# Performance work log

Measured on AMD Instinct MI355X. Metric: run time of the kernel, lower is better.

The kernel has to match this reference:

```python
import jax, jax.numpy as jnp
import numpy as np

NUM_NODES = 500000
DIM = 128
BATCH = 131072
MOMENTUM = 0.9


def setup_inputs() -> dict:
    key = jax.random.key(0)
    ks = jax.random.split(key, 6)
    s = 1.0 / np.sqrt(DIM)
    return {
        "hidden": jax.random.normal(ks[0], (NUM_NODES, DIM), jnp.float32),
        "variance": jnp.ones((NUM_NODES, DIM), jnp.float32),
        "idx": jnp.arange(BATCH, dtype=jnp.int64 if jax.config.jax_enable_x64 else jnp.int32),
        "new_repr": jax.random.normal(ks[1], (BATCH, DIM), jnp.float32),
        "W_ih": jax.random.normal(ks[2], (3 * DIM, DIM), jnp.float32) * s,
        "W_hh": jax.random.normal(ks[3], (3 * DIM, DIM), jnp.float32) * s,
        "b_ih": jax.random.normal(ks[4], (3 * DIM,), jnp.float32) * s,
        "b_hh": jax.random.normal(ks[5], (3 * DIM,), jnp.float32) * s,
    }


def _gru_cell(x, h, W_ih, W_hh, b_ih, b_hh):
    # torch GRUCell gate layout: [reset | update | new], each of size DIM
    gi = x @ W_ih.T + b_ih          # [B, 3*DIM]
    gh = h @ W_hh.T + b_hh          # [B, 3*DIM]
    gi_r, gi_z, gi_n = jnp.split(gi, 3, axis=-1)
    gh_r, gh_z, gh_n = jnp.split(gh, 3, axis=-1)
    r = jax.nn.sigmoid(gi_r + gh_r)
    z = jax.nn.sigmoid(gi_z + gh_z)
    n = jnp.tanh(gi_n + r * gh_n)
    return (1.0 - z) * n + z * h


def reference(hidden, variance, idx, new_repr, W_ih, W_hh, b_ih, b_hh):
    h_prev = hidden[idx]                                   # gather [B, DIM]
    h_new = _gru_cell(new_repr, h_prev, W_ih, W_hh, b_ih, b_hh)
    delta = h_new - h_prev
    var_new = MOMENTUM * variance[idx] + (1.0 - MOMENTUM) * delta * delta
    hidden_out = hidden.at[idx].set(h_new)                 # scatter write
    variance_out = variance.at[idx].set(var_new)
    return jnp.stack([hidden_out, variance_out])           # [2, N, DIM]
```

## Files before the change

### kernel.cpp

```cpp
#include <hip/hip_runtime.h>
#include <hip/hip_bf16.h>
#include <cstdint>
#include <cstddef>

#define NUM_NODES 500000
#define DIM 128
#define BATCH 131072
#define NBLK (NUM_NODES / 32)

typedef __attribute__((ext_vector_type(8))) short short8;
typedef __attribute__((ext_vector_type(4))) short short4_t;
typedef __attribute__((ext_vector_type(4))) float f32x4;

static __device__ __forceinline__ short f2bf(float f) {
    unsigned u = __builtin_bit_cast(unsigned, f);
    u += 0x7fffu + ((u >> 16) & 1u);
    return (short)(u >> 16);
}
static __device__ __forceinline__ float bf2f(short s) {
    unsigned u = ((unsigned)(unsigned short)s) << 16;
    return __builtin_bit_cast(float, u);
}
static __device__ __forceinline__ f32x4 ntl(const float* p) {
    return __builtin_nontemporal_load((const f32x4*)p);
}
static __device__ __forceinline__ void nts(float* p, f32x4 v) {
    __builtin_nontemporal_store(v, (f32x4*)p);
}

__global__ void k_init(int* __restrict__ inv,
                       unsigned char* __restrict__ mask,
                       const float* __restrict__ Wih,
                       const float* __restrict__ Whh,
                       short* __restrict__ WbIH,
                       short* __restrict__ WbHH) {
    int i = blockIdx.x * blockDim.x + threadIdx.x;
    if (i < NUM_NODES) {
        if (inv)  inv[i] = -1;
        if (mask) mask[i] = 0;
    }
    if (i < 3 * DIM * DIM) {
        WbIH[i] = f2bf(Wih[i]);
        WbHH[i] = f2bf(Whh[i]);
    }
}

__global__ void k_scatter(int* __restrict__ inv, unsigned char* __restrict__ mask,
                          const int* __restrict__ idx) {
    int i = blockIdx.x * blockDim.x + threadIdx.x;
    if (i < BATCH) {
        int n = idx[i];
        if (inv)  inv[n] = i;
        if (mask) mask[n] = 1;
    }
}

__global__ void __launch_bounds__(512)
k_stream(const float* __restrict__ hidden,
         const float* __restrict__ variance,
         const int*   __restrict__ inv,
         const float* __restrict__ xg,
         const short* __restrict__ WbIH,
         const short* __restrict__ WbHH,
         const float* __restrict__ b_ih,
         const float* __restrict__ b_hh,
         float* __restrict__ out0,
         float* __restrict__ out1) {
    __shared__ __align__(16) char smem[26112];
    short (*Xb)[136] = (short(*)[136])smem;
    short (*Hb)[136] = (short(*)[136])(smem + 8704);
    short (*Vb)[136] = (short(*)[136])(smem + 17408);
    short (*Hn)[136] = (short(*)[136])smem;
    __shared__ int rinfo[32];
    __shared__ int hasUpd;

    const int t  = threadIdx.x;
    const int pb = (int)(((unsigned)blockIdx.x * 4099u) % 15625u);
    const int rb = pb * 32;

    if (t == 0) hasUpd = 0;
    if (t < 32) rinfo[t] = inv[rb + t];
    __syncthreads();
    if (t < 32 && rinfo[t] >= 0) hasUpd = 1;
    __syncthreads();

    if (!hasUpd) {
        #pragma unroll
        for (int jj = 0; jj < 2; ++jj) {
            int j = t + jj * 512;
            size_t off = (size_t)rb * DIM + j * 4;
            f32x4 h = ntl(hidden + off);
            f32x4 v = ntl(variance + off);
            nts(out0 + off, h);
            nts(out1 + off, v);
        }
        return;
    }

    #pragma unroll
    for (int jj = 0; jj < 2; ++jj) {
        int j = t + jj * 512;
        int row = j >> 5, c4 = j & 31;
        size_t off = (size_t)(rb + row) * DIM + c4 * 4;
        f32x4 hv = ntl(hidden + off);
        f32x4 vv = ntl(variance + off);
        int iv = rinfo[row];
        f32x4 xv = {0.f, 0.f, 0.f, 0.f};
        if (iv >= 0) {
            xv = ntl(xg + (size_t)iv * DIM + c4 * 4);
        } else {
            nts(out0 + off, hv);
            nts(out1 + off, vv);
        }
        short4_t xs, hs, vs;
        xs.x = f2bf(xv.x); xs.y = f2bf(xv.y); xs.z = f2bf(xv.z); xs.w = f2bf(xv.w);
        hs.x = f2bf(hv.x); hs.y = f2bf(hv.y); hs.z = f2bf(hv.z); hs.w = f2bf(hv.w);
        vs.x = f2bf(vv.x); vs.y = f2bf(vv.y); vs.z = f2bf(vv.z); vs.w = f2bf(vv.w);
        *(short4_t*)&Xb[row][c4 * 4] = xs;
        *(short4_t*)&Hb[row][c4 * 4] = hs;
        *(short4_t*)&Vb[row][c4 * 4] = vs;
    }
    __syncthreads();

    const int w  = t >> 6;
    const int l  = t & 63;
    const int c  = l & 15;
    const int gq = l >> 4;

    float sr[2][4], sz[2][4], gin[2][4], ghn[2][4];

    #pragma unroll
    for (int th = 0; th < 3; ++th) {
        f32x4 acc[2][2] = {};
        const int o = w * 16 + th * 128 + c;
        #pragma unroll
        for (int ks = 0; ks < 4; ++ks) {
            const int k0 = ks * 32 + gq * 8;
            const short8 aX0 = *(const short8*)&Xb[c][k0];
            const short8 aX1 = *(const short8*)&Xb[16 + c][k0];
            const short8 aH0 = *(const short8*)&Hb[c][k0];
            const short8 aH1 = *(const short8*)&Hb[16 + c][k0];
            const short8 bi = *(const short8*)(WbIH + (size_t)o * DIM + k0);
            const short8 bh = *(const short8*)(WbHH + (size_t)o * DIM + k0);
            acc[0][0] = __builtin_amdgcn_mfma_f32_16x16x32_bf16(aX0, bi, acc[0][0], 0, 0, 0);
            acc[1][0] = __builtin_amdgcn_mfma_f32_16x16x32_bf16(aX1, bi, acc[1][0], 0, 0, 0);
            acc[0][1] = __builtin_amdgcn_mfma_f32_16x16x32_bf16(aH0, bh, acc[0][1], 0, 0, 0);
            acc[1][1] = __builtin_amdgcn_mfma_f32_16x16x32_bf16(aH1, bh, acc[1][1], 0, 0, 0);
        }
        #pragma unroll
        for (int mt = 0; mt < 2; ++mt)
            #pragma unroll
            for (int r = 0; r < 4; ++r) {
                if (th == 0) sr[mt][r]  = acc[mt][0][r] + acc[mt][1][r];
                if (th == 1) sz[mt][r]  = acc[mt][0][r] + acc[mt][1][r];
                if (th == 2) { gin[mt][r] = acc[mt][0][r]; ghn[mt][r] = acc[mt][1][r]; }
            }
    }
    __syncthreads();

    const int d = w * 16 + c;
    const float bs_r = b_ih[d]       + b_hh[d];
    const float bs_z = b_ih[d + 128] + b_hh[d + 128];
    const float bi_n = b_ih[d + 256];
    const float bh_n = b_hh[d + 256];

    #pragma unroll
    for (int mt = 0; mt < 2; ++mt) {
        #pragma unroll
        for (int r = 0; r < 4; ++r) {
            const int m = mt * 16 + gq * 4 + r;
            float s_r  = sr[mt][r] + bs_r;
            float s_z  = sz[mt][r] + bs_z;
            float gi_n = gin[mt][r] + bi_n;
            float gh_n = ghn[mt][r] + bh_n;
            float rg = 1.f / (1.f + __expf(-s_r));
            float zg = 1.f / (1.f + __expf(-s_z));
            float aa = gi_n + rg * gh_n;
            float n  = 1.f - 2.f / (__expf(2.f * aa) + 1.f);
            float h  = bf2f(Hb[m][d]);
            Hn[m][d] = f2bf((1.f - zg) * n + zg * h);
        }
    }
    __syncthreads();

    #pragma unroll
    for (int jj = 0; jj < 2; ++jj) {
        int j = t + jj * 512;
        int row = j >> 5, c4 = j & 31;
        if (rinfo[row] < 0) continue;
        size_t off = (size_t)(rb + row) * DIM + c4 * 4;
        short4_t hns = *(short4_t*)&Hn[row][c4 * 4];
        short4_t hs  = *(short4_t*)&Hb[row][c4 * 4];
        short4_t vs  = *(short4_t*)&Vb[row][c4 * 4];
        f32x4 hn, var;
        hn.x = bf2f(hns.x); hn.y = bf2f(hns.y); hn.z = bf2f(hns.z); hn.w = bf2f(hns.w);
        float dx = hn.x - bf2f(hs.x), dy = hn.y - bf2f(hs.y);
        float dz = hn.z - bf2f(hs.z), dw = hn.w - bf2f(hs.w);
        var.x = 0.9f * bf2f(vs.x) + 0.1f * dx * dx;
        var.y = 0.9f * bf2f(vs.y) + 0.1f * dy * dy;
        var.z = 0.9f * bf2f(vs.z) + 0.1f * dz * dz;
        var.w = 0.9f * bf2f(vs.w) + 0.1f * dw * dw;
        nts(out0 + off, hn);
        nts(out1 + off, var);
    }
}

__global__ void __launch_bounds__(256)
k_copy(const float* __restrict__ hidden,
       const float* __restrict__ variance,
       const unsigned char* __restrict__ mask,
       float* __restrict__ out0,
       float* __restrict__ out1) {
    int gid = blockIdx.x * 256 + threadIdx.x;
    int row = gid >> 4;
    int c8  = gid & 15;
    if (mask && mask[row]) return;
    size_t off = (size_t)row * DIM + c8 * 8;
    f32x4 a0 = *(const f32x4*)(hidden + off);
    f32x4 a1 = *(const f32x4*)(hidden + off + 4);
    f32x4 b0 = *(const f32x4*)(variance + off);
    f32x4 b1 = *(const f32x4*)(variance + off + 4);
    *(f32x4*)(out0 + off)     = a0;
    *(f32x4*)(out0 + off + 4) = a1;
    *(f32x4*)(out1 + off)     = b0;
    *(f32x4*)(out1 + off + 4) = b1;
}

__global__ void __launch_bounds__(512)
k_gru(const float* __restrict__ hidden,
      const float* __restrict__ variance,
      const int*   __restrict__ idx,
      const float* __restrict__ xg,
      const short* __restrict__ WbIH,
      const short* __restrict__ WbHH,
      const float* __restrict__ b_ih,
      const float* __restrict__ b_hh,
      float* __restrict__ out0,
      float* __restrict__ out1) {
    __shared__ __align__(16) char smem[26112];
    short (*Xb)[136] = (short(*)[136])smem;
    short (*Hb)[136] = (short(*)[136])(smem + 8704);
    short (*Vb)[136] = (short(*)[136])(smem + 17408);
    short (*Hn)[136] = (short(*)[136])smem;

    const int t  = threadIdx.x;
    const int rb = blockIdx.x * 32;

    #pragma unroll
    for (int jj = 0; jj < 2; ++jj) {
        int j = t + jj * 512;
        int row = j >> 5, c4 = j & 31;
        int node = idx[rb + row];
        f32x4 xv = *(const f32x4*)(xg + (size_t)(rb + row) * DIM + c4 * 4);
        f32x4 hv = *(const f32x4*)(hidden + (size_t)node * DIM + c4 * 4);
        f32x4 vv = *(const f32x4*)(variance + (size_t)node * DIM + c4 * 4);
        short4_t xs, hs, vs;
        xs.x = f2bf(xv.x); xs.y = f2bf(xv.y); xs.z = f2bf(xv.z); xs.w = f2bf(xv.w);
        hs.x = f2bf(hv.x); hs.y = f2bf(hv.y); hs.z = f2bf(hv.z); hs.w = f2bf(hv.w);
        vs.x = f2bf(vv.x); vs.y = f2bf(vv.y); vs.z = f2bf(vv.z); vs.w = f2bf(vv.w);
        *(short4_t*)&Xb[row][c4 * 4] = xs;
        *(short4_t*)&Hb[row][c4 * 4] = hs;
        *(short4_t*)&Vb[row][c4 * 4] = vs;
    }
    __syncthreads();

    const int w  = t >> 6;
    const int l  = t & 63;
    const int c  = l & 15;
    const int gq = l >> 4;

    f32x4 acc[2][3][2] = {};
    #pragma unroll
    for (int ks = 0; ks < 4; ++ks) {
        const int k0 = ks * 32 + gq * 8;
        short8 a[2][2];
        a[0][0] = *(const short8*)&Xb[c][k0];
        a[1][0] = *(const short8*)&Xb[16 + c][k0];
        a[0][1] = *(const short8*)&Hb[c][k0];
        a[1][1] = *(const short8*)&Hb[16 + c][k0];
        #pragma unroll
        for (int th = 0; th < 3; ++th) {
            const int o = w * 16 + th * 128 + c;
            const short8 bi = *(const short8*)(WbIH + (size_t)o * DIM + k0);
            const short8 bh = *(const short8*)(WbHH + (size_t)o * DIM + k0);
            #pragma unroll
            for (int mt = 0; mt < 2; ++mt) {
                acc[mt][th][0] = __builtin_amdgcn_mfma_f32_16x16x32_bf16(a[mt][0], bi, acc[mt][th][0], 0, 0, 0);
                acc[mt][th][1] = __builtin_amdgcn_mfma_f32_16x16x32_bf16(a[mt][1], bh, acc[mt][th][1], 0, 0, 0);
            }
        }
    }
    __syncthreads();

    const int d = w * 16 + c;
    const float bs_r = b_ih[d]       + b_hh[d];
    const float bs_z = b_ih[d + 128] + b_hh[d + 128];
    const float bi_n = b_ih[d + 256];
    const float bh_n = b_hh[d + 256];
    #pragma unroll
    for (int mt = 0; mt < 2; ++mt) {
        #pragma unroll
        for (int r = 0; r < 4; ++r) {
            const int m = mt * 16 + gq * 4 + r;
            float s_r  = acc[mt][0][0][r] + acc[mt][0][1][r] + bs_r;
            float s_z  = acc[mt][1][0][r] + acc[mt][1][1][r] + bs_z;
            float gi_n = acc[mt][2][0][r] + bi_n;
            float gh_n = acc[mt][2][1][r] + bh_n;
            float rg = 1.f / (1.f + __expf(-s_r));
            float zg = 1.f / (1.f + __expf(-s_z));
            float aa = gi_n + rg * gh_n;
            float n  = 1.f - 2.f / (__expf(2.f * aa) + 1.f);
            float h  = bf2f(Hb[m][d]);
            Hn[m][d] = f2bf((1.f - zg) * n + zg * h);
        }
    }
    __syncthreads();

    #pragma unroll
    for (int jj = 0; jj < 2; ++jj) {
        int j = t + jj * 512;
        int row = j >> 5, c4 = j & 31;
        int node = idx[rb + row];
        size_t off = (size_t)node * DIM + c4 * 4;
        short4_t hns = *(short4_t*)&Hn[row][c4 * 4];
        short4_t hs  = *(short4_t*)&Hb[row][c4 * 4];
        short4_t vs  = *(short4_t*)&Vb[row][c4 * 4];
        f32x4 hn, var;
        hn.x = bf2f(hns.x); hn.y = bf2f(hns.y); hn.z = bf2f(hns.z); hn.w = bf2f(hns.w);
        float dx = hn.x - bf2f(hs.x), dy = hn.y - bf2f(hs.y);
        float dz = hn.z - bf2f(hs.z), dw = hn.w - bf2f(hs.w);
        var.x = 0.9f * bf2f(vs.x) + 0.1f * dx * dx;
        var.y = 0.9f * bf2f(vs.y) + 0.1f * dy * dy;
        var.z = 0.9f * bf2f(vs.z) + 0.1f * dz * dz;
        var.w = 0.9f * bf2f(vs.w) + 0.1f * dw * dw;
        *(f32x4*)(out0 + off) = hn;
        *(f32x4*)(out1 + off) = var;
    }
}

extern "C" void kernel_launch(void* const* d_in, const int* in_sizes, int n_in,
                              void* d_out, int out_size, void* d_ws, size_t ws_size,
                              hipStream_t stream) {
    const float* hidden   = (const float*)d_in[0];
    const float* variance = (const float*)d_in[1];
    const int*   idx      = (const int*)d_in[2];
    const float* x        = (const float*)d_in[3];
    const float* Wih      = (const float*)d_in[4];
    const float* Whh      = (const float*)d_in[5];
    const float* bih      = (const float*)d_in[6];
    const float* bhh      = (const float*)d_in[7];
    float* out0 = (float*)d_out;
    float* out1 = out0 + (size_t)NUM_NODES * DIM;

    const size_t invB  = (size_t)NUM_NODES * 4;
    const size_t maskB = (size_t)NUM_NODES;
    const size_t wB    = (size_t)3 * DIM * DIM * 2;

    const bool full = ws_size >= invB + 2 * wB;
    const bool mid  = !full && ws_size >= maskB + 16 + 2 * wB;

    if (full) {
        int*   inv  = (int*)d_ws;
        short* WbIH = (short*)((char*)d_ws + invB);
        short* WbHH = WbIH + 3 * DIM * DIM;
        k_init<<<(NUM_NODES + 255) / 256, 256, 0, stream>>>(
            inv, nullptr, Wih, Whh, WbIH, WbHH);
        k_scatter<<<BATCH / 256, 256, 0, stream>>>(inv, nullptr, idx);
        k_stream<<<NBLK, 512, 0, stream>>>(hidden, variance, inv, x,
                                           WbIH, WbHH, bih, bhh, out0, out1);
    } else if (mid) {
        unsigned char* mask = (unsigned char*)d_ws;
        short* WbIH = (short*)((char*)d_ws + ((maskB + 15) & ~size_t(15)));
        short* WbHH = WbIH + 3 * DIM * DIM;
        k_init<<<(NUM_NODES + 255) / 256, 256, 0, stream>>>(
            nullptr, mask, Wih, Whh, WbIH, WbHH);
        k_scatter<<<BATCH / 256, 256, 0, stream>>>(nullptr, mask, idx);
        k_copy<<<(NUM_NODES * 16) / 256, 256, 0, stream>>>(
            hidden, variance, mask, out0, out1);
        k_gru<<<BATCH / 32, 512, 0, stream>>>(hidden, variance, idx, x,
                                              WbIH, WbHH, bih, bhh, out0, out1);
    } else {
        short* WbIH = (short*)d_ws;
        short* WbHH = WbIH + 3 * DIM * DIM;
        k_init<<<(NUM_NODES + 255) / 256, 256, 0, stream>>>(
            nullptr, nullptr, Wih, Whh, WbIH, WbHH);
        k_copy<<<(NUM_NODES * 16) / 256, 256, 0, stream>>>(
            hidden, variance, nullptr, out0, out1);
        k_gru<<<BATCH / 32, 512, 0, stream>>>(hidden, variance, idx, x,
                                              WbIH, WbHH, bih, bhh, out0, out1);
    }
}
```

Before: 248.0 us.

## Issue hidden/variance loads before sync and keep them in registers

```diff
diff --git a/kernel.cpp b/kernel.cpp
--- a/kernel.cpp
+++ b/kernel.cpp
@@ -66,33 +66,35 @@
          const float* __restrict__ b_hh,
          float* __restrict__ out0,
          float* __restrict__ out1) {
-    __shared__ __align__(16) char smem[26112];
-    short (*Xb)[136] = (short(*)[136])smem;
-    short (*Hb)[136] = (short(*)[136])(smem + 8704);
-    short (*Vb)[136] = (short(*)[136])(smem + 17408);
-    short (*Hn)[136] = (short(*)[136])smem;
+    __shared__ __align__(16) short Xb[32][136];
+    __shared__ __align__(16) short Hb[32][136];
+    short (*Hn)[136] = Xb;
     __shared__ int rinfo[32];
-    __shared__ int hasUpd;
 
     const int t  = threadIdx.x;
+    const int l  = t & 63;
     const int pb = (int)(((unsigned)blockIdx.x * 4099u) % 15625u);
     const int rb = pb * 32;
 
-    if (t == 0) hasUpd = 0;
+    f32x4 hv[2], vv[2];
+    #pragma unroll
+    for (int jj = 0; jj < 2; ++jj) {
+        int j = t + jj * 512;
+        size_t off = (size_t)rb * DIM + j * 4;
+        hv[jj] = ntl(hidden + off);
+        vv[jj] = ntl(variance + off);
+    }
     if (t < 32) rinfo[t] = inv[rb + t];
     __syncthreads();
-    if (t < 32 && rinfo[t] >= 0) hasUpd = 1;
-    __syncthreads();
+    const bool hasUpd = __any(rinfo[l & 31] >= 0);
 
     if (!hasUpd) {
         #pragma unroll
         for (int jj = 0; jj < 2; ++jj) {
             int j = t + jj * 512;
             size_t off = (size_t)rb * DIM + j * 4;
-            f32x4 h = ntl(hidden + off);
-            f32x4 v = ntl(variance + off);
-            nts(out0 + off, h);
-            nts(out1 + off, v);
+            nts(out0 + off, hv[jj]);
+            nts(out1 + off, vv[jj]);
         }
         return;
     }
@@ -102,28 +104,23 @@
         int j = t + jj * 512;
         int row = j >> 5, c4 = j & 31;
         size_t off = (size_t)(rb + row) * DIM + c4 * 4;
-        f32x4 hv = ntl(hidden + off);
-        f32x4 vv = ntl(variance + off);
         int iv = rinfo[row];
         f32x4 xv = {0.f, 0.f, 0.f, 0.f};
         if (iv >= 0) {
             xv = ntl(xg + (size_t)iv * DIM + c4 * 4);
         } else {
-            nts(out0 + off, hv);
-            nts(out1 + off, vv);
-        }
-        short4_t xs, hs, vs;
-        xs.x = f2bf(xv.x); xs.y = f2bf(xv.y); xs.z = f2bf(xv.z); xs.w = f2bf(xv.w);
-        hs.x = f2bf(hv.x); hs.y = f2bf(hv.y); hs.z = f2bf(hv.z); hs.w = f2bf(hv.w);
-        vs.x = f2bf(vv.x); vs.y = f2bf(vv.y); vs.z = f2bf(vv.z); vs.w = f2bf(vv.w);
+            nts(out0 + off, hv[jj]);
+            nts(out1 + off, vv[jj]);
+        }
+        short4_t xs, hs;
+        xs.x = f2bf(xv.x);    xs.y = f2bf(xv.y);    xs.z = f2bf(xv.z);    xs.w = f2bf(xv.w);
+        hs.x = f2bf(hv[jj].x); hs.y = f2bf(hv[jj].y); hs.z = f2bf(hv[jj].z); hs.w = f2bf(hv[jj].w);
         *(short4_t*)&Xb[row][c4 * 4] = xs;
         *(short4_t*)&Hb[row][c4 * 4] = hs;
-        *(short4_t*)&Vb[row][c4 * 4] = vs;
     }
     __syncthreads();
 
     const int w  = t >> 6;
-    const int l  = t & 63;
     const int c  = l & 15;
     const int gq = l >> 4;
 
@@ -190,16 +187,14 @@
         if (rinfo[row] < 0) continue;
         size_t off = (size_t)(rb + row) * DIM + c4 * 4;
         short4_t hns = *(short4_t*)&Hn[row][c4 * 4];
-        short4_t hs  = *(short4_t*)&Hb[row][c4 * 4];
-        short4_t vs  = *(short4_t*)&Vb[row][c4 * 4];
         f32x4 hn, var;
         hn.x = bf2f(hns.x); hn.y = bf2f(hns.y); hn.z = bf2f(hns.z); hn.w = bf2f(hns.w);
-        float dx = hn.x - bf2f(hs.x), dy = hn.y - bf2f(hs.y);
-        float dz = hn.z - bf2f(hs.z), dw = hn.w - bf2f(hs.w);
-        var.x = 0.9f * bf2f(vs.x) + 0.1f * dx * dx;
-        var.y = 0.9f * bf2f(vs.y) + 0.1f * dy * dy;
-        var.z = 0.9f * bf2f(vs.z) + 0.1f * dz * dz;
-        var.w = 0.9f * bf2f(vs.w) + 0.1f * dw * dw;
+        float dx = hn.x - hv[jj].x, dy = hn.y - hv[jj].y;
+        float dz = hn.z - hv[jj].z, dw = hn.w - hv[jj].w;
+        var.x = 0.9f * vv[jj].x + 0.1f * dx * dx;
+        var.y = 0.9f * vv[jj].y + 0.1f * dy * dy;
+        var.z = 0.9f * vv[jj].z + 0.1f * dz * dz;
+        var.w = 0.9f * vv[jj].w + 0.1f * dw * dw;
         nts(out0 + off, hn);
         nts(out1 + off, var);
     }
```

After: 295.0 us. 19.0% more time.
